# Kernel tuning notes

Hardware: AMD Instinct MI355X
Metric: run time of the kernel (lower is better)

## Reference

```python
import math
import jax, jax.numpy as jnp
import numpy as np

G_RATIO = 0.5
TB_FACTOR = 1e-3


def _expand(x):
    # x: [B,H,W]; 3x3 all-ones-except-center neighbor conv (same filter for every sample)
    k = jnp.ones((1, 1, 3, 3), x.dtype).at[0, 0, 1, 1].set(0.0)
    y = jax.lax.conv_general_dilated(x[:, None], k, (1, 1), 'SAME')
    return y[:, 0]


def _st_softmax_noexp(val):
    # straight-through normalized selection over flattened map
    B = val.shape[0]
    v = val.reshape(B, -1)
    y = v / v.sum(-1, keepdims=True)
    ind = jnp.argmax(y, -1)
    y_hard = jax.nn.one_hot(ind, y.shape[-1], dtype=y.dtype)
    y = y + jax.lax.stop_gradient(y_hard - y)
    return y.reshape(val.shape)


def _heuristic(gm):
    # gm: [B,H,W] one-hot goal maps -> Chebyshev + tb*Euclidean distance field
    B, H, W = gm.shape
    loc = jnp.stack(jnp.meshgrid(jnp.arange(H), jnp.arange(W), indexing='ij'), 0).astype(gm.dtype)  # [2,H,W]
    loc_e = loc.reshape(2, -1)[None]                      # [1,2,HW]
    goal_loc = jnp.einsum('kij,bij->bk', loc, gm)[:, :, None]  # [B,2,1]
    d = jnp.abs(loc_e - goal_loc)                         # [B,2,HW]
    h = d.sum(1) - d.min(1)
    euc = jnp.sqrt(((loc_e - goal_loc) ** 2).sum(1))
    return (h + TB_FACTOR * euc).reshape(B, H, W)


def _forward_core(cost_maps, start_maps, goal_maps, obstacles_maps):
    cm, sm, gm, om = cost_maps[:, 0], start_maps[:, 0], goal_maps[:, 0], obstacles_maps[:, 0]
    B, H, W = cm.shape
    h = _heuristic(gm) + cm
    goal_idx = jnp.argmax(gm.reshape(B, -1), -1)
    parents0 = jnp.broadcast_to(goal_idx[:, None].astype(cm.dtype), (B, H * W))
    inv_sqrt = 1.0 / math.sqrt(W)
    Tmax = W * W

    def step(carry, i):
        g, open_m, hist, parents, done, t = carry
        f = G_RATIO * g + (1.0 - G_RATIO) * h
        f_exp = jnp.exp(-f * inv_sqrt) * open_m
        snm = _st_softmax_noexp(f_exp)
        dist = (snm * gm).sum((1, 2), keepdims=True)
        unsolved = (dist < 1e-8).astype(cm.dtype)
        hist_n = jnp.clip(hist + snm, 0.0, 1.0)
        open_n = jnp.clip(open_m - unsolved * snm, 0.0, 1.0)
        nb = _expand(snm) * om
        g2 = _expand((g + cm) * snm)
        idx = ((1.0 - open_n) * (1.0 - hist_n) + open_n * (g > g2).astype(cm.dtype)) * nb
        idx = jax.lax.stop_gradient(idx)
        g_n = jax.lax.stop_gradient(g2 * idx + g * (1.0 - idx))
        open_n = jax.lax.stop_gradient(jnp.clip(open_n + idx, 0.0, 1.0))
        idx_f = idx.reshape(B, -1)
        new_par = jnp.argmax(snm.reshape(B, -1), -1)[:, None].astype(cm.dtype)
        par_n = new_par * idx_f + parents * (1.0 - idx_f)
        done_n = jnp.all(unsolved == 0)
        sel = lambda new, old: jnp.where(done, old, new)  # emulate the torch early break
        carry_n = (sel(g_n, g), sel(open_n, open_m), sel(hist_n, hist), sel(par_n, parents),
                   jnp.logical_or(done, done_n), jnp.where(done, t, i))
        return carry_n, None

    init = (jnp.zeros_like(sm), sm, jnp.zeros_like(sm), parents0,
            jnp.array(False), jnp.array(0, jnp.int32))
    (g, open_m, hist, parents, done, t), _ = jax.lax.scan(
        step, init, jnp.arange(Tmax, dtype=jnp.int32))
    return hist[:, None], parents, t


def _backtrack(goal_maps, parents, t):
    gm = goal_maps[:, 0]
    B, H, W = gm.shape
    par_i = parents.astype(jnp.int32)
    goal_f = gm.reshape(B, -1).astype(jnp.int32)
    loc = (par_i * goal_f).sum(-1)
    rng = jnp.arange(B)

    def bt(i, val):
        path, loc = val
        path = path.at[rng, loc].set(1)
        loc = jnp.take_along_axis(par_i, loc[:, None], -1)[:, 0]
        return (path, loc)

    path, _ = jax.lax.fori_loop(0, t, bt, (goal_f, loc))
    return path.reshape(B, 1, H, W)


def setup_inputs() -> dict:
    key = jax.random.key(0)
    k1, k2, k3, k4 = jax.random.split(key, 4)
    B, H, W = 16, 32, 32
    cost_maps = jax.random.uniform(k1, (B, 1, H, W), dtype=jnp.float32)
    sidx = jax.random.randint(k2, (B,), 0, H * W)
    gidx = jax.random.randint(k3, (B,), 0, H * W)
    gidx = jnp.where(gidx == sidx, (gidx + 1) % (H * W), gidx)
    start_maps = jax.nn.one_hot(sidx, H * W, dtype=jnp.float32).reshape(B, 1, H, W)
    goal_maps = jax.nn.one_hot(gidx, H * W, dtype=jnp.float32).reshape(B, 1, H, W)
    obstacles_maps = (jax.random.uniform(k4, (B, 1, H, W)) > 0.05).astype(jnp.float32)
    obstacles_maps = jnp.clip(obstacles_maps + start_maps + goal_maps, 0.0, 1.0)
    return {'cost_maps': cost_maps, 'start_maps': start_maps,
            'goal_maps': goal_maps, 'obstacles_maps': obstacles_maps}


def reference(cost_maps, start_maps, goal_maps, obstacles_maps):
    histories, parents, t = _forward_core(cost_maps, start_maps, goal_maps, obstacles_maps)
    path_maps = _backtrack(goal_maps, parents, t)
    return histories, path_maps
```

## Files before the change

### kernel.cpp

```cpp
#include <hip/hip_runtime.h>
#include <math.h>

#define HH 32
#define WW 32
#define HW 1024
#define NB 16
#define TMAXS 1024

#pragma clang fp contract(off)

__device__ __forceinline__ float keyval(float g, float h) {
#pragma clang fp contract(off)
  const float INV = 0.17677669529663687f;
  float f = 0.5f * g + 0.5f * h;
  return expf(-f * INV);
}

extern "C" __global__ void __launch_bounds__(64) astar_fwd(
    const float* __restrict__ cm_g, const float* __restrict__ sm_g,
    const float* __restrict__ gm_g, const float* __restrict__ om_g,
    float* __restrict__ out, int* __restrict__ meta) {
#pragma clang fp contract(off)
  const int b = blockIdx.x;
  const int lane = threadIdx.x;
  __shared__ __align__(16) float key[HW];
  __shared__ __align__(16) float gS[HW];
  __shared__ __align__(16) float hS[HW];
  __shared__ __align__(16) float cmS[HW];
  __shared__ unsigned short par[HW];
  __shared__ unsigned char flg[HW];

  const float* cm = cm_g + b * HW;
  const float* sm = sm_g + b * HW;
  const float* gm = gm_g + b * HW;
  const float* om = om_g + b * HW;

  int gi = -1, si = -1;
#pragma unroll
  for (int q = 0; q < 4; ++q) {
    const int base = q * 256 + lane * 4;
    float4 c4 = *(const float4*)(cm + base);
    float4 s4 = *(const float4*)(sm + base);
    float4 g4 = *(const float4*)(gm + base);
    float4 o4 = *(const float4*)(om + base);
    *(float4*)(cmS + base) = c4;
    float sv[4] = {s4.x, s4.y, s4.z, s4.w};
    float gv[4] = {g4.x, g4.y, g4.z, g4.w};
    float ov[4] = {o4.x, o4.y, o4.z, o4.w};
#pragma unroll
    for (int j = 0; j < 4; ++j) {
      flg[base + j] = (ov[j] > 0.5f) ? 1 : 0;
      if (gv[j] > 0.5f) gi = base + j;
      if (sv[j] > 0.5f) si = base + j;
    }
  }
#pragma unroll
  for (int m = 32; m >= 1; m >>= 1) {
    int og = __shfl_xor(gi, m, 64);
    int os = __shfl_xor(si, m, 64);
    gi = (og > gi) ? og : gi;
    si = (os > si) ? os : si;
  }
  const int goal = gi;
  const int start = si;

  const float gr = (float)(goal >> 5), gc = (float)(goal & 31);
#pragma unroll
  for (int q = 0; q < 4; ++q) {
    const int base = q * 256 + lane * 4;
#pragma unroll
    for (int j = 0; j < 4; ++j) {
      const int cell = base + j;
      const float rr = (float)(cell >> 5), cc = (float)(cell & 31);
      const float dr = fabsf(rr - gr), dc = fabsf(cc - gc);
      const float h0 = (dr + dc) - fminf(dr, dc);
      const float euc = sqrtf(dr * dr + dc * dc);
      const float t1 = 0.001f * euc;
      const float hh = h0 + t1;
      hS[cell] = hh + cmS[cell];
      gS[cell] = 0.0f;
      key[cell] = 0.0f;
      par[cell] = (unsigned short)goal;
    }
  }
  __syncthreads();
  if (lane == 0) {
    flg[start] = (unsigned char)(flg[start] | 2);
    key[start] = keyval(0.0f, hS[start]);
  }
  __syncthreads();

  int s_b = TMAXS - 1;
  for (int step = 0; step < TMAXS; ++step) {
    float best = -1.0f;
    int bi = 0;
#pragma unroll
    for (int q = 0; q < 4; ++q) {
      const int base = q * 256 + lane * 4;
      float4 k4 = *(const float4*)(key + base);
      if (k4.x > best) { best = k4.x; bi = base; }
      if (k4.y > best) { best = k4.y; bi = base + 1; }
      if (k4.z > best) { best = k4.z; bi = base + 2; }
      if (k4.w > best) { best = k4.w; bi = base + 3; }
    }
#pragma unroll
    for (int m = 32; m >= 1; m >>= 1) {
      float ov = __shfl_xor(best, m, 64);
      int oi = __shfl_xor(bi, m, 64);
      if (ov > best || (ov == best && oi < bi)) { best = ov; bi = oi; }
    }
    const int sel = bi;
    const bool isg = (sel == goal);
    const float g2 = gS[sel] + cmS[sel];
    const int r = sel >> 5, c = sel & 31;

    if (lane < 8) {
      const int k = (lane < 4) ? lane : lane + 1;
      const int nr = r + k / 3 - 1, nc = c + k % 3 - 1;
      if (nr >= 0 && nr < HH && nc >= 0 && nc < WW) {
        const int n = (nr << 5) | nc;
        const unsigned char f = flg[n];
        if (f & 1) {
          const bool open = (f & 2) != 0, hb = (f & 4) != 0;
          if ((!open && !hb) || (open && gS[n] > g2)) {
            gS[n] = g2;
            flg[n] = (unsigned char)(f | 2);
            par[n] = (unsigned short)sel;
            key[n] = keyval(g2, hS[n]);
          }
        }
      }
    }
    if (lane == 0) {
      if (isg) {
        flg[sel] = (unsigned char)(flg[sel] | 4);
      } else {
        flg[sel] = (unsigned char)((flg[sel] | 4) & ~2);
        key[sel] = 0.0f;
      }
    }
    __syncthreads();
    if (isg) { s_b = step; break; }
  }

#pragma unroll
  for (int q = 0; q < 4; ++q) {
    const int base = q * 256 + lane * 4;
    float4 h4, p4;
    h4.x = (flg[base + 0] & 4) ? 1.0f : 0.0f;
    h4.y = (flg[base + 1] & 4) ? 1.0f : 0.0f;
    h4.z = (flg[base + 2] & 4) ? 1.0f : 0.0f;
    h4.w = (flg[base + 3] & 4) ? 1.0f : 0.0f;
    p4.x = (float)par[base + 0];
    p4.y = (float)par[base + 1];
    p4.z = (float)par[base + 2];
    p4.w = (float)par[base + 3];
    *(float4*)(out + b * HW + base) = h4;
    *(float4*)(out + NB * HW + b * HW + base) = p4;
  }
  if (lane == 0) meta[b] = s_b;
}

extern "C" __global__ void __launch_bounds__(64) astar_bt(
    const float* __restrict__ gm_g, float* __restrict__ out,
    const int* __restrict__ meta) {
  const int b = blockIdx.x;
  const int lane = threadIdx.x;
  __shared__ unsigned short par[HW];
  __shared__ float path[HW];

  float* pout = out + NB * HW + b * HW;
  const float* gm = gm_g + b * HW;

  int gi = -1;
#pragma unroll
  for (int q = 0; q < 4; ++q) {
    const int base = q * 256 + lane * 4;
    float4 g4 = *(const float4*)(gm + base);
    float4 p4 = *(const float4*)(pout + base);
    par[base + 0] = (unsigned short)p4.x;
    par[base + 1] = (unsigned short)p4.y;
    par[base + 2] = (unsigned short)p4.z;
    par[base + 3] = (unsigned short)p4.w;
    path[base + 0] = 0.0f;
    path[base + 1] = 0.0f;
    path[base + 2] = 0.0f;
    path[base + 3] = 0.0f;
    if (g4.x > 0.5f) gi = base;
    if (g4.y > 0.5f) gi = base + 1;
    if (g4.z > 0.5f) gi = base + 2;
    if (g4.w > 0.5f) gi = base + 3;
  }
#pragma unroll
  for (int m = 32; m >= 1; m >>= 1) {
    int og = __shfl_xor(gi, m, 64);
    gi = (og > gi) ? og : gi;
  }
  const int goal = gi;

  int t = 0;
  for (int i = 0; i < NB; ++i) {
    int s = meta[i];
    t = (s > t) ? s : t;
  }
  __syncthreads();
  if (lane == 0) {
    path[goal] = 1.0f;
    int loc = par[goal];
    for (int i = 0; i < t; ++i) {
      if (path[loc] == 1.0f) break;
      path[loc] = 1.0f;
      loc = par[loc];
    }
  }
  __syncthreads();
#pragma unroll
  for (int q = 0; q < 4; ++q) {
    const int base = q * 256 + lane * 4;
    float4 o4;
    o4.x = path[base + 0];
    o4.y = path[base + 1];
    o4.z = path[base + 2];
    o4.w = path[base + 3];
    *(float4*)(pout + base) = o4;
  }
}

extern "C" void kernel_launch(void* const* d_in, const int* in_sizes, int n_in,
                              void* d_out, int out_size, void* d_ws,
                              size_t ws_size, hipStream_t stream) {
  const float* cm = (const float*)d_in[0];
  const float* sm = (const float*)d_in[1];
  const float* gm = (const float*)d_in[2];
  const float* om = (const float*)d_in[3];
  float* out = (float*)d_out;
  int* meta = (int*)d_ws;
  hipLaunchKernelGGL(astar_fwd, dim3(NB), dim3(64), 0, stream, cm, sm, gm, om,
                     out, meta);
  hipLaunchKernelGGL(astar_bt, dim3(NB), dim3(64), 0, stream, gm, out, meta);
}
```

Baseline: 93.48 us.

## Fuse forward search and backtrack, pack key+index into 64-bit argmax with DPP

Merges the forward A* kernel and the backtrack kernel into one launch, so the second launch and the round trip of parents through global memory go away. The argmax packs the float key as a double with the inverted cell index in its low bits, and reduces it with DPP row operations and a readlane instead of a shuffle-based pair compare. The per-step __syncthreads become wave barriers, and cell state is grouped into a float4 per cell. Backtracking marks path cells with a high bit in par and is no longer bounded by the max step across batches, which could change results if a parent cycle or step-limit case behaves differently from the reference.

```diff
diff --git a/kernel.cpp b/kernel.cpp
--- a/kernel.cpp
+++ b/kernel.cpp
@@ -7,7 +7,7 @@
 #define NB 16
 #define TMAXS 1024
 
-#pragma clang fp contract(off)
+typedef unsigned long long ull;
 
 __device__ __forceinline__ float keyval(float g, float h) {
 #pragma clang fp contract(off)
@@ -16,213 +16,172 @@
   return expf(-f * INV);
 }
 
-extern "C" __global__ void __launch_bounds__(64) astar_fwd(
+template <int CTRL>
+__device__ __forceinline__ double dpp_fmax64(double x) {
+  ull u = (ull)__double_as_longlong(x);
+  int lo = (int)(unsigned)u;
+  int hi = (int)(unsigned)(u >> 32);
+  int lo2 = __builtin_amdgcn_update_dpp(0, lo, CTRL, 0xF, 0xF, false);
+  int hi2 = __builtin_amdgcn_update_dpp(0, hi, CTRL, 0xF, 0xF, false);
+  double y = __longlong_as_double(
+      (long long)(((ull)(unsigned)hi2 << 32) | (unsigned)lo2));
+  return fmax(x, y);
+}
+
+extern "C" __global__ void __launch_bounds__(64) astar_fused(
     const float* __restrict__ cm_g, const float* __restrict__ sm_g,
     const float* __restrict__ gm_g, const float* __restrict__ om_g,
-    float* __restrict__ out, int* __restrict__ meta) {
+    float* __restrict__ out) {
 #pragma clang fp contract(off)
   const int b = blockIdx.x;
   const int lane = threadIdx.x;
-  __shared__ __align__(16) float key[HW];
-  __shared__ __align__(16) float gS[HW];
-  __shared__ __align__(16) float hS[HW];
-  __shared__ __align__(16) float cmS[HW];
-  __shared__ unsigned short par[HW];
-  __shared__ unsigned char flg[HW];
+
+  __shared__ __align__(16) ull key2[HW];
+  __shared__ __align__(16) float4 gch[HW];
+  __shared__ unsigned int flg[HW];
+  __shared__ unsigned int par[HW];
 
   const float* cm = cm_g + b * HW;
   const float* sm = sm_g + b * HW;
   const float* gm = gm_g + b * HW;
   const float* om = om_g + b * HW;
 
+  float cml[16], oml[16];
   int gi = -1, si = -1;
 #pragma unroll
-  for (int q = 0; q < 4; ++q) {
-    const int base = q * 256 + lane * 4;
-    float4 c4 = *(const float4*)(cm + base);
-    float4 s4 = *(const float4*)(sm + base);
-    float4 g4 = *(const float4*)(gm + base);
-    float4 o4 = *(const float4*)(om + base);
-    *(float4*)(cmS + base) = c4;
-    float sv[4] = {s4.x, s4.y, s4.z, s4.w};
-    float gv[4] = {g4.x, g4.y, g4.z, g4.w};
-    float ov[4] = {o4.x, o4.y, o4.z, o4.w};
-#pragma unroll
-    for (int j = 0; j < 4; ++j) {
-      flg[base + j] = (ov[j] > 0.5f) ? 1 : 0;
-      if (gv[j] > 0.5f) gi = base + j;
-      if (sv[j] > 0.5f) si = base + j;
-    }
+  for (int q = 0; q < 16; ++q) {
+    const int cell = q * 64 + lane;
+    const float c = cm[cell], s = sm[cell], g = gm[cell], o = om[cell];
+    cml[q] = c;
+    oml[q] = o;
+    if (g > 0.5f) gi = cell;
+    if (s > 0.5f) si = cell;
   }
 #pragma unroll
   for (int m = 32; m >= 1; m >>= 1) {
-    int og = __shfl_xor(gi, m, 64);
-    int os = __shfl_xor(si, m, 64);
+    const int og = __shfl_xor(gi, m, 64);
+    const int os = __shfl_xor(si, m, 64);
     gi = (og > gi) ? og : gi;
     si = (os > si) ? os : si;
   }
-  const int goal = gi;
-  const int start = si;
+  const int goal = gi, start = si;
 
-  const float gr = (float)(goal >> 5), gc = (float)(goal & 31);
+  const float grf = (float)(goal >> 5), gcf = (float)(goal & 31);
 #pragma unroll
-  for (int q = 0; q < 4; ++q) {
-    const int base = q * 256 + lane * 4;
+  for (int q = 0; q < 16; ++q) {
+    const int cell = q * 64 + lane;
+    const float rr = (float)(cell >> 5), cc = (float)(cell & 31);
+    const float dr = fabsf(rr - grf), dc = fabsf(cc - gcf);
+    const float h0 = (dr + dc) - fminf(dr, dc);
+    const float euc = sqrtf(dr * dr + dc * dc);
+    const float t1 = 0.001f * euc;
+    const float hh = h0 + t1;
+    const float hf = hh + cml[q];
+    gch[cell] = make_float4(0.0f, cml[q], cml[q], hf);
+    unsigned f = (oml[q] > 0.5f) ? 1u : 0u;
+    ull pk = (ull)(1023 - cell);
+    if (cell == start) {
+      f |= 2u;
+      pk |= (ull)__double_as_longlong((double)keyval(0.0f, hf));
+    }
+    flg[cell] = f;
+    par[cell] = (unsigned)goal;
+    key2[cell] = pk;
+  }
+
+  int dro = 0, dco = 0;
+  if (lane < 8) {
+    const int k = (lane < 4) ? lane : lane + 1;
+    dro = k / 3 - 1;
+    dco = k % 3 - 1;
+  }
+  const float* gchf = (const float*)gch;
+  __builtin_amdgcn_wave_barrier();
+
+#pragma unroll 1
+  for (int step = 0; step < TMAXS; ++step) {
+    double s[8];
 #pragma unroll
-    for (int j = 0; j < 4; ++j) {
-      const int cell = base + j;
-      const float rr = (float)(cell >> 5), cc = (float)(cell & 31);
-      const float dr = fabsf(rr - gr), dc = fabsf(cc - gc);
-      const float h0 = (dr + dc) - fminf(dr, dc);
-      const float euc = sqrtf(dr * dr + dc * dc);
-      const float t1 = 0.001f * euc;
-      const float hh = h0 + t1;
-      hS[cell] = hh + cmS[cell];
-      gS[cell] = 0.0f;
-      key[cell] = 0.0f;
-      par[cell] = (unsigned short)goal;
+    for (int q = 0; q < 8; ++q) {
+      const ulonglong2 v = *(const ulonglong2*)&key2[q * 128 + lane * 2];
+      s[q] = fmax(__longlong_as_double((long long)v.x),
+                  __longlong_as_double((long long)v.y));
+    }
+    const double t0 = fmax(s[0], s[1]), t1 = fmax(s[2], s[3]);
+    const double t2 = fmax(s[4], s[5]), t3 = fmax(s[6], s[7]);
+    double mm = fmax(fmax(t0, t1), fmax(t2, t3));
+
+    mm = dpp_fmax64<0x111>(mm);
+    mm = dpp_fmax64<0x112>(mm);
+    mm = dpp_fmax64<0x114>(mm);
+    mm = dpp_fmax64<0x118>(mm);
+    mm = dpp_fmax64<0x142>(mm);
+    mm = dpp_fmax64<0x143>(mm);
+    const int lo63 =
+        __builtin_amdgcn_readlane((int)(unsigned)(ull)__double_as_longlong(mm), 63);
+    const int sel = 1023 - (lo63 & 1023);
+
+    if (sel == goal) {
+      if (lane == 0) flg[goal] |= 4u;
+      break;
+    }
+
+    if (lane < 9) {
+      if (lane < 8) {
+        const int nr = (sel >> 5) + dro, nc = (sel & 31) + dco;
+        if ((unsigned)nr < 32u && (unsigned)nc < 32u) {
+          const int n = (nr << 5) | nc;
+          const unsigned f = flg[n];
+          const float4 v = gch[n];
+          const float g2 = gchf[4 * sel + 2];
+          const bool upd =
+              (f & 1u) && (((f & 6u) == 0u) || (((f & 2u) != 0u) && (v.x > g2)));
+          if (upd) {
+            gch[n] = make_float4(g2, v.y, g2 + v.y, v.w);
+            flg[n] = f | 2u;
+            par[n] = (unsigned)sel;
+            const float kk = keyval(g2, v.w);
+            key2[n] = ((ull)__double_as_longlong((double)kk)) | (ull)(1023 - n);
+          }
+        }
+      } else {
+        const unsigned fs = flg[sel];
+        flg[sel] = (fs | 4u) & ~2u;
+        key2[sel] = (ull)(1023 - sel);
+      }
+    }
+    __builtin_amdgcn_wave_barrier();
+  }
+
+  __builtin_amdgcn_wave_barrier();
+  if (lane == 0) {
+    const unsigned pv = par[goal];
+    par[goal] = pv | 0x80000000u;
+    unsigned loc = pv & 1023u;
+#pragma unroll 1
+    for (int i = 0; i < HW; ++i) {
+      const unsigned v = par[loc];
+      if (v & 0x80000000u) break;
+      par[loc] = v | 0x80000000u;
+      loc = v & 1023u;
     }
   }
-  __syncthreads();
-  if (lane == 0) {
-    flg[start] = (unsigned char)(flg[start] | 2);
-    key[start] = keyval(0.0f, hS[start]);
-  }
-  __syncthreads();
-
-  int s_b = TMAXS - 1;
-  for (int step = 0; step < TMAXS; ++step) {
-    float best = -1.0f;
-    int bi = 0;
-#pragma unroll
-    for (int q = 0; q < 4; ++q) {
-      const int base = q * 256 + lane * 4;
-      float4 k4 = *(const float4*)(key + base);
-      if (k4.x > best) { best = k4.x; bi = base; }
-      if (k4.y > best) { best = k4.y; bi = base + 1; }
-      if (k4.z > best) { best = k4.z; bi = base + 2; }
-      if (k4.w > best) { best = k4.w; bi = base + 3; }
-    }
-#pragma unroll
-    for (int m = 32; m >= 1; m >>= 1) {
-      float ov = __shfl_xor(best, m, 64);
-      int oi = __shfl_xor(bi, m, 64);
-      if (ov > best || (ov == best && oi < bi)) { best = ov; bi = oi; }
-    }
-    const int sel = bi;
-    const bool isg = (sel == goal);
-    const float g2 = gS[sel] + cmS[sel];
-    const int r = sel >> 5, c = sel & 31;
-
-    if (lane < 8) {
-      const int k = (lane < 4) ? lane : lane + 1;
-      const int nr = r + k / 3 - 1, nc = c + k % 3 - 1;
-      if (nr >= 0 && nr < HH && nc >= 0 && nc < WW) {
-        const int n = (nr << 5) | nc;
-        const unsigned char f = flg[n];
-        if (f & 1) {
-          const bool open = (f & 2) != 0, hb = (f & 4) != 0;
-          if ((!open && !hb) || (open && gS[n] > g2)) {
-            gS[n] = g2;
-            flg[n] = (unsigned char)(f | 2);
-            par[n] = (unsigned short)sel;
-            key[n] = keyval(g2, hS[n]);
-          }
-        }
-      }
-    }
-    if (lane == 0) {
-      if (isg) {
-        flg[sel] = (unsigned char)(flg[sel] | 4);
-      } else {
-        flg[sel] = (unsigned char)((flg[sel] | 4) & ~2);
-        key[sel] = 0.0f;
-      }
-    }
-    __syncthreads();
-    if (isg) { s_b = step; break; }
-  }
+  __builtin_amdgcn_wave_barrier();
 
 #pragma unroll
   for (int q = 0; q < 4; ++q) {
     const int base = q * 256 + lane * 4;
-    float4 h4, p4;
-    h4.x = (flg[base + 0] & 4) ? 1.0f : 0.0f;
-    h4.y = (flg[base + 1] & 4) ? 1.0f : 0.0f;
-    h4.z = (flg[base + 2] & 4) ? 1.0f : 0.0f;
-    h4.w = (flg[base + 3] & 4) ? 1.0f : 0.0f;
-    p4.x = (float)par[base + 0];
-    p4.y = (float)par[base + 1];
-    p4.z = (float)par[base + 2];
-    p4.w = (float)par[base + 3];
-    *(float4*)(out + b * HW + base) = h4;
-    *(float4*)(out + NB * HW + b * HW + base) = p4;
-  }
-  if (lane == 0) meta[b] = s_b;
-}
-
-extern "C" __global__ void __launch_bounds__(64) astar_bt(
-    const float* __restrict__ gm_g, float* __restrict__ out,
-    const int* __restrict__ meta) {
-  const int b = blockIdx.x;
-  const int lane = threadIdx.x;
-  __shared__ unsigned short par[HW];
-  __shared__ float path[HW];
-
-  float* pout = out + NB * HW + b * HW;
-  const float* gm = gm_g + b * HW;
-
-  int gi = -1;
-#pragma unroll
-  for (int q = 0; q < 4; ++q) {
-    const int base = q * 256 + lane * 4;
-    float4 g4 = *(const float4*)(gm + base);
-    float4 p4 = *(const float4*)(pout + base);
-    par[base + 0] = (unsigned short)p4.x;
-    par[base + 1] = (unsigned short)p4.y;
-    par[base + 2] = (unsigned short)p4.z;
-    par[base + 3] = (unsigned short)p4.w;
-    path[base + 0] = 0.0f;
-    path[base + 1] = 0.0f;
-    path[base + 2] = 0.0f;
-    path[base + 3] = 0.0f;
-    if (g4.x > 0.5f) gi = base;
-    if (g4.y > 0.5f) gi = base + 1;
-    if (g4.z > 0.5f) gi = base + 2;
-    if (g4.w > 0.5f) gi = base + 3;
-  }
-#pragma unroll
-  for (int m = 32; m >= 1; m >>= 1) {
-    int og = __shfl_xor(gi, m, 64);
-    gi = (og > gi) ? og : gi;
-  }
-  const int goal = gi;
-
-  int t = 0;
-  for (int i = 0; i < NB; ++i) {
-    int s = meta[i];
-    t = (s > t) ? s : t;
-  }
-  __syncthreads();
-  if (lane == 0) {
-    path[goal] = 1.0f;
-    int loc = par[goal];
-    for (int i = 0; i < t; ++i) {
-      if (path[loc] == 1.0f) break;
-      path[loc] = 1.0f;
-      loc = par[loc];
-    }
-  }
-  __syncthreads();
-#pragma unroll
-  for (int q = 0; q < 4; ++q) {
-    const int base = q * 256 + lane * 4;
-    float4 o4;
-    o4.x = path[base + 0];
-    o4.y = path[base + 1];
-    o4.z = path[base + 2];
-    o4.w = path[base + 3];
-    *(float4*)(pout + base) = o4;
+    float4 hv, pv;
+    hv.x = (flg[base + 0] & 4u) ? 1.0f : 0.0f;
+    hv.y = (flg[base + 1] & 4u) ? 1.0f : 0.0f;
+    hv.z = (flg[base + 2] & 4u) ? 1.0f : 0.0f;
+    hv.w = (flg[base + 3] & 4u) ? 1.0f : 0.0f;
+    pv.x = (par[base + 0] >> 31) ? 1.0f : 0.0f;
+    pv.y = (par[base + 1] >> 31) ? 1.0f : 0.0f;
+    pv.z = (par[base + 2] >> 31) ? 1.0f : 0.0f;
+    pv.w = (par[base + 3] >> 31) ? 1.0f : 0.0f;
+    *(float4*)(out + b * HW + base) = hv;
+    *(float4*)(out + NB * HW + b * HW + base) = pv;
   }
 }
 
@@ -234,8 +193,6 @@
   const float* gm = (const float*)d_in[2];
   const float* om = (const float*)d_in[3];
   float* out = (float*)d_out;
-  int* meta = (int*)d_ws;
-  hipLaunchKernelGGL(astar_fwd, dim3(NB), dim3(64), 0, stream, cm, sm, gm, om,
-                     out, meta);
-  hipLaunchKernelGGL(astar_bt, dim3(NB), dim3(64), 0, stream, gm, out, meta);
+  hipLaunchKernelGGL(astar_fused, dim3(NB), dim3(64), 0, stream, cm, sm, gm,
+                     om, out);
 }
```

Measured after the change: 79.87 us. 1.17x faster.
